# Performance work log

Hardware: AMD Instinct MI355X
Metric: run time of the kernel (lower is better)

The kernel has to match this reference:

```python
import jax, jax.numpy as jnp
import numpy as np

B, L, DM, H, DK, DV = 8, 1024, 512, 8, 64, 64
LN_EPS = 1e-5

def setup_inputs() -> dict:
    key = jax.random.key(0)
    ks = jax.random.split(key, 8)
    s_in = 1.0 / np.sqrt(DM)
    return {
        "q": jax.random.normal(ks[0], (B, L, DM), jnp.float32),
        "k": jax.random.normal(ks[1], (B, L, DM), jnp.float32),
        "v": jax.random.normal(ks[2], (B, L, DM), jnp.float32),
        "Wq": jax.random.normal(ks[3], (DM, H * DK), jnp.float32) * s_in,
        "bq": jnp.zeros((H * DK,), jnp.float32),
        "Wk": jax.random.normal(ks[4], (DM, H * DK), jnp.float32) * s_in,
        "bk": jnp.zeros((H * DK,), jnp.float32),
        "Wv": jax.random.normal(ks[5], (DM, H * DV), jnp.float32) * s_in,
        "bv": jnp.zeros((H * DV,), jnp.float32),
        "Wmap": jax.random.normal(ks[6], (2 * DK, 1), jnp.float32) * (1.0 / np.sqrt(2 * DK)),
        "bmap": jnp.zeros((1,), jnp.float32),
        "Wfc": jax.random.normal(ks[7], (H * DV, DM), jnp.float32) * (1.0 / np.sqrt(H * DV)),
        "bfc": jnp.zeros((DM,), jnp.float32),
        "ln_scale": jnp.ones((DM,), jnp.float32),
        "ln_bias": jnp.zeros((DM,), jnp.float32),
    }

def reference(q, k, v, Wq, bq, Wk, bk, Wv, bv, Wmap, bmap, Wfc, bfc, ln_scale, ln_bias):
    sz_b, len_q, _ = q.shape
    len_k = k.shape[1]
    residual = q
    # projections -> (H, B, L, d)
    qh = (q @ Wq + bq).reshape(sz_b, len_q, H, DK).transpose(2, 0, 1, 3)
    kh = (k @ Wk + bk).reshape(sz_b, len_k, H, DK).transpose(2, 0, 1, 3)
    vh = (v @ Wv + bv).reshape(sz_b, len_k, H, DV).transpose(2, 0, 1, 3)
    # additive score: Linear(concat(q,k)) == q@Wmap[:DK] + k@Wmap[DK:] + b
    # (avoids materializing the (H*B, Lq, Lk, 2*DK) concat; same math)
    sq = qh @ Wmap[:DK, 0]   # (H, B, Lq)
    sk = kh @ Wmap[DK:, 0]   # (H, B, Lk)
    scores = sq[..., :, None] + sk[..., None, :] + bmap[0]  # (H, B, Lq, Lk)
    attn = jax.nn.softmax(scores, axis=-1)
    out = jnp.einsum('hbqk,hbkd->hbqd', attn, vh)            # (H, B, Lq, DV)
    out = out.transpose(1, 2, 0, 3).reshape(sz_b, len_q, H * DV)
    out = out @ Wfc + bfc + residual
    mu = out.mean(-1, keepdims=True)
    var = out.var(-1, keepdims=True)
    out = (out - mu) / jnp.sqrt(var + LN_EPS) * ln_scale + ln_bias
    return out, attn.reshape(H * sz_b, len_q, len_k)
```

## Files before the change

kernel.cpp:

```cpp
#include <hip/hip_runtime.h>
#include <cstdint>
#include <cstddef>

#define B 8
#define L 1024
#define DM 512
#define H 8
#define DK 64
#define DV 64
#define LN_EPS 1e-5f

#define U_OFF    0
#define CK_OFF   4096
#define SK_OFF   8192
#define P_OFF    73728
#define PART_OFF 139264
#define CTX_OFF  270336
#define OBP_OFF  274432

#define OUT_ELEMS  ((size_t)B * L * DM)

typedef float f4 __attribute__((ext_vector_type(4)));

__global__ __launch_bounds__(64) void k_prep(const float* __restrict__ Wk,
                                             const float* __restrict__ bk,
                                             const float* __restrict__ Wmap,
                                             float* __restrict__ ws) {
    __shared__ float wm[DK];
    int t = threadIdx.x;
    wm[t] = Wmap[DK + t];
    __syncthreads();
    int h = t >> 3, part = t & 7;
#pragma unroll
    for (int i = 0; i < 8; ++i) {
        int dm = blockIdx.x * 8 + i;
        const float* row = Wk + (size_t)dm * (H * DK) + h * DK + part * 8;
        float s = 0.f;
#pragma unroll
        for (int d = 0; d < 8; ++d) s += row[d] * wm[part * 8 + d];
        s += __shfl_xor(s, 1, 64);
        s += __shfl_xor(s, 2, 64);
        s += __shfl_xor(s, 4, 64);
        if (part == 0) ws[U_OFF + dm * H + h] = s;
    }
    if (blockIdx.x == 0) {
        const float* rb = bk + h * DK + part * 8;
        float s = 0.f;
#pragma unroll
        for (int d = 0; d < 8; ++d) s += rb[d] * wm[part * 8 + d];
        s += __shfl_xor(s, 1, 64);
        s += __shfl_xor(s, 2, 64);
        s += __shfl_xor(s, 4, 64);
        if (part == 0) ws[CK_OFF + h] = s;
    }
}

__global__ __launch_bounds__(256) void k_sk(const float* __restrict__ k,
                                            float* __restrict__ ws) {
    int wave = threadIdx.x >> 6, lane = threadIdx.x & 63;
    int row = blockIdx.x * 4 + wave;
    int b = row >> 10, l = row & 1023;
    const float* krow = k + (size_t)row * DM;
    const float* u = ws + U_OFF;
    float acc[8] = {0, 0, 0, 0, 0, 0, 0, 0};
#pragma unroll
    for (int s = 0; s < 8; ++s) {
        int dm = s * 64 + lane;
        float kv = krow[dm];
        const float4 ua = *(const float4*)(u + dm * 8);
        const float4 ub = *(const float4*)(u + dm * 8 + 4);
        acc[0] += kv * ua.x; acc[1] += kv * ua.y;
        acc[2] += kv * ua.z; acc[3] += kv * ua.w;
        acc[4] += kv * ub.x; acc[5] += kv * ub.y;
        acc[6] += kv * ub.z; acc[7] += kv * ub.w;
    }
#pragma unroll
    for (int off = 32; off > 0; off >>= 1) {
#pragma unroll
        for (int h = 0; h < 8; ++h) acc[h] += __shfl_xor(acc[h], off, 64);
    }
    float vout = 0.f;
#pragma unroll
    for (int h = 0; h < 8; ++h) if (lane == h) vout = acc[h];
    if (lane < 8)
        ws[SK_OFF + ((size_t)(lane * B + b)) * L + l] = vout + ws[CK_OFF + lane];
}

__global__ __launch_bounds__(256) void k_softmax(float* __restrict__ ws) {
    int hb = blockIdx.x, t = threadIdx.x;
    int wave = t >> 6, lane = t & 63;
    const float4 s4 = *(const float4*)&ws[SK_OFF + (size_t)hb * L + t * 4];
    __shared__ float sred[4];
    __shared__ float bc[1];
    float m = fmaxf(fmaxf(s4.x, s4.y), fmaxf(s4.z, s4.w));
#pragma unroll
    for (int off = 32; off > 0; off >>= 1) m = fmaxf(m, __shfl_xor(m, off, 64));
    if (lane == 0) sred[wave] = m;
    __syncthreads();
    if (t == 0) bc[0] = fmaxf(fmaxf(sred[0], sred[1]), fmaxf(sred[2], sred[3]));
    __syncthreads();
    m = bc[0];
    float e0 = expf(s4.x - m), e1 = expf(s4.y - m), e2 = expf(s4.z - m), e3 = expf(s4.w - m);
    float s = e0 + e1 + e2 + e3;
#pragma unroll
    for (int off = 32; off > 0; off >>= 1) s += __shfl_xor(s, off, 64);
    __syncthreads();
    if (lane == 0) sred[wave] = s;
    __syncthreads();
    if (t == 0) bc[0] = sred[0] + sred[1] + sred[2] + sred[3];
    __syncthreads();
    float inv = 1.f / bc[0];
    float4 p4 = {e0 * inv, e1 * inv, e2 * inv, e3 * inv};
    *(float4*)&ws[P_OFF + (size_t)hb * L + t * 4] = p4;
}

__global__ __launch_bounds__(512) void k_vbar(const float* __restrict__ v,
                                              float* __restrict__ ws) {
    __shared__ float ps[H * 256];
    int blk = blockIdx.x;
    int chunk = blk & 7, b = (blk >> 3) & 7, js = blk >> 6;
    for (int idx = threadIdx.x; idx < H * 256; idx += 512) {
        int hh = idx >> 8, jj = idx & 255;
        ps[idx] = ws[P_OFF + ((size_t)(hh * B + b)) * L + js * 256 + jj];
    }
    __syncthreads();
    int h = threadIdx.x >> 6, dml = threadIdx.x & 63;
    int dm = chunk * 64 + dml;
    const float* vb0 = v + ((size_t)b * L + js * 256) * DM + dm;
    const float* ph = &ps[h * 256];
    float acc = 0.f;
#pragma unroll 4
    for (int jj = 0; jj < 256; ++jj) acc += ph[jj] * vb0[(size_t)jj * DM];
    ws[PART_OFF + ((size_t)((js * H + h) * B + b)) * DM + dm] = acc;
}

__global__ __launch_bounds__(256) void k_ctx(const float* __restrict__ Wv,
                                             const float* __restrict__ bv,
                                             float* __restrict__ ws) {
    __shared__ float vb[DM];
    __shared__ float red[4][64];
    int hb = blockIdx.x;
    int h = hb >> 3, b = hb & 7;
#pragma unroll
    for (int it = 0; it < 2; ++it) {
        int dm = threadIdx.x + it * 256;
        float s = 0.f;
#pragma unroll
        for (int js = 0; js < 4; ++js)
            s += ws[PART_OFF + ((size_t)((js * H + h) * B + b)) * DM + dm];
        vb[dm] = s;
    }
    __syncthreads();
    int w = threadIdx.x >> 6, d = threadIdx.x & 63;
    float acc = 0.f;
#pragma unroll 4
    for (int i = 0; i < 128; ++i) {
        int dm = w * 128 + i;
        acc += vb[dm] * Wv[(size_t)dm * (H * DV) + h * DV + d];
    }
    red[w][d] = acc;
    __syncthreads();
    if (w == 0) {
        float r = red[0][d] + red[1][d] + red[2][d] + red[3][d] + bv[h * DV + d];
        ws[CTX_OFF + (size_t)b * DM + h * DV + d] = r;
    }
}

__global__ __launch_bounds__(512) void k_obase(const float* __restrict__ Wfc,
                                               float* __restrict__ ws) {
    __shared__ float cxs[64];
    int b = blockIdx.x & 7, ms = blockIdx.x >> 3;
    if (threadIdx.x < 64)
        cxs[threadIdx.x] = ws[CTX_OFF + (size_t)b * DM + ms * 64 + threadIdx.x];
    __syncthreads();
    int n = threadIdx.x;
    float acc = 0.f;
#pragma unroll 4
    for (int m = 0; m < 64; ++m)
        acc += cxs[m] * Wfc[(size_t)(ms * 64 + m) * DM + n];
    ws[OBP_OFF + (size_t)(ms * B + b) * DM + n] = acc;
}

__global__ __launch_bounds__(256) void k_out(const float* __restrict__ q,
                                             const float* __restrict__ bfc,
                                             const float* __restrict__ lns,
                                             const float* __restrict__ lnb,
                                             const float* __restrict__ ws,
                                             float* __restrict__ out) {
    __shared__ float obf[DM];
    int b = blockIdx.x >> 8;
    for (int i = threadIdx.x; i < DM; i += 256) {
        float s = bfc[i];
#pragma unroll
        for (int ms = 0; ms < 8; ++ms)
            s += ws[OBP_OFF + (size_t)(ms * B + b) * DM + i];
        obf[i] = s;
    }
    __syncthreads();
    int wave = threadIdx.x >> 6, lane = threadIdx.x & 63;
    int row = blockIdx.x * 4 + wave;
    const float* qr = q + (size_t)row * DM;
    int d0 = lane * 8;
    float4 a = *(const float4*)(qr + d0);
    float4 c = *(const float4*)(qr + d0 + 4);
    float x[8] = {a.x + obf[d0], a.y + obf[d0 + 1], a.z + obf[d0 + 2], a.w + obf[d0 + 3],
                  c.x + obf[d0 + 4], c.y + obf[d0 + 5], c.z + obf[d0 + 6], c.w + obf[d0 + 7]};
    float sum = 0.f, sq = 0.f;
#pragma unroll
    for (int i = 0; i < 8; ++i) { sum += x[i]; sq += x[i] * x[i]; }
#pragma unroll
    for (int off = 32; off > 0; off >>= 1) {
        sum += __shfl_xor(sum, off, 64);
        sq  += __shfl_xor(sq,  off, 64);
    }
    float mu = sum * (1.f / DM);
    float var = sq * (1.f / DM) - mu * mu;
    float inv = rsqrtf(var + LN_EPS);
    float4 sa = *(const float4*)(lns + d0);
    float4 sc = *(const float4*)(lns + d0 + 4);
    float4 ba = *(const float4*)(lnb + d0);
    float4 bb = *(const float4*)(lnb + d0 + 4);
    float sarr[8] = {sa.x, sa.y, sa.z, sa.w, sc.x, sc.y, sc.z, sc.w};
    float barr[8] = {ba.x, ba.y, ba.z, ba.w, bb.x, bb.y, bb.z, bb.w};
    float y[8];
#pragma unroll
    for (int i = 0; i < 8; ++i) y[i] = (x[i] - mu) * inv * sarr[i] + barr[i];
    float4 o0 = {y[0], y[1], y[2], y[3]};
    float4 o1 = {y[4], y[5], y[6], y[7]};
    *(float4*)(out + (size_t)row * DM + d0) = o0;
    *(float4*)(out + (size_t)row * DM + d0 + 4) = o1;
}

__global__ __launch_bounds__(256) void k_attn(const float* __restrict__ ws,
                                              float* __restrict__ out) {
    int hb = blockIdx.x >> 6;
    int ic = blockIdx.x & 63;
    f4 pv = *(const f4*)&ws[P_OFF + (size_t)hb * L + threadIdx.x * 4];
    float* base = out + OUT_ELEMS + ((size_t)hb * L + (size_t)ic * 16) * L + threadIdx.x * 4;
#pragma unroll
    for (int r = 0; r < 16; ++r)
        __builtin_nontemporal_store(pv, (f4*)(base + (size_t)r * L));
}

extern "C" void kernel_launch(void* const* d_in, const int* in_sizes, int n_in,
                              void* d_out, int out_size, void* d_ws, size_t ws_size,
                              hipStream_t stream) {
    const float* q    = (const float*)d_in[0];
    const float* k    = (const float*)d_in[1];
    const float* v    = (const float*)d_in[2];
    const float* Wk   = (const float*)d_in[5];
    const float* bk   = (const float*)d_in[6];
    const float* Wv   = (const float*)d_in[7];
    const float* bv   = (const float*)d_in[8];
    const float* Wmap = (const float*)d_in[9];
    const float* Wfc  = (const float*)d_in[11];
    const float* bfc  = (const float*)d_in[12];
    const float* lns  = (const float*)d_in[13];
    const float* lnb  = (const float*)d_in[14];
    float* out = (float*)d_out;
    float* ws  = (float*)d_ws;

    hipLaunchKernelGGL(k_prep,    dim3(64),   dim3(64),  0, stream, Wk, bk, Wmap, ws);
    hipLaunchKernelGGL(k_sk,      dim3(2048), dim3(256), 0, stream, k, ws);
    hipLaunchKernelGGL(k_softmax, dim3(64),   dim3(256), 0, stream, ws);
    hipLaunchKernelGGL(k_vbar,    dim3(256),  dim3(512), 0, stream, v, ws);
    hipLaunchKernelGGL(k_ctx,     dim3(64),   dim3(256), 0, stream, Wv, bv, ws);
    hipLaunchKernelGGL(k_obase,   dim3(64),   dim3(512), 0, stream, Wfc, ws);
    hipLaunchKernelGGL(k_out,     dim3(2048), dim3(256), 0, stream, q, bfc, lns, lnb, ws, out);
    hipLaunchKernelGGL(k_attn,    dim3(4096), dim3(256), 0, stream, ws, out);
}
```

Before: 118.2 us.

## Fuse all stages into one cooperative kernel overlapping attention-map stores

Replaces the eight separate launches with a single cooperative persistent kernel of 512 blocks that uses grid-wide syncs between stages. The large attention-map writes are split into tasks and handed to otherwise idle blocks during the small serial stages (v-bar, ctx, obase), so the bandwidth-bound output stream overlaps the dependent compute chain. Softmax is now recomputed per task instead of being read from a stored probability buffer, the constant key-bias term that cancels in softmax is dropped, and fast __expf replaces expf. In exchange the kernel pays for five grid syncs, repeats the row reductions in every task, and needs all blocks to be co-resident.

```diff
diff --git a/kernel.cpp b/kernel.cpp
--- a/kernel.cpp
+++ b/kernel.cpp
@@ -1,245 +1,266 @@
 #include <hip/hip_runtime.h>
+#include <hip/hip_cooperative_groups.h>
 #include <cstdint>
 #include <cstddef>
+
+namespace cg = cooperative_groups;
 
 #define B 8
 #define L 1024
 #define DM 512
 #define H 8
-#define DK 64
-#define DV 64
 #define LN_EPS 1e-5f
 
 #define U_OFF    0
-#define CK_OFF   4096
 #define SK_OFF   8192
-#define P_OFF    73728
-#define PART_OFF 139264
-#define CTX_OFF  270336
-#define OBP_OFF  274432
-
-#define OUT_ELEMS  ((size_t)B * L * DM)
+#define PART_OFF 73728
+#define CTX_OFF  204800
+#define OBP_OFF  208896
+
+#define OUT_ELEMS ((size_t)B * L * DM)
+
+#define NBLK 512
+#define NTHR 256
 
 typedef float f4 __attribute__((ext_vector_type(4)));
 
-__global__ __launch_bounds__(64) void k_prep(const float* __restrict__ Wk,
-                                             const float* __restrict__ bk,
-                                             const float* __restrict__ Wmap,
-                                             float* __restrict__ ws) {
-    __shared__ float wm[DK];
-    int t = threadIdx.x;
-    wm[t] = Wmap[DK + t];
+__device__ __forceinline__ float wave_max(float m) {
+#pragma unroll
+    for (int off = 32; off > 0; off >>= 1) m = fmaxf(m, __shfl_xor(m, off, 64));
+    return m;
+}
+__device__ __forceinline__ float wave_sum(float s) {
+#pragma unroll
+    for (int off = 32; off > 0; off >>= 1) s += __shfl_xor(s, off, 64);
+    return s;
+}
+
+__device__ __forceinline__ void attn_task(int task, const float* __restrict__ ws,
+                                          float* __restrict__ out,
+                                          float* rmax, float* rsum,
+                                          int t, int wave, int lane) {
+    int hb = task >> 6, ic = task & 63;
+    float4 s4 = *(const float4*)&ws[SK_OFF + (size_t)hb * L + t * 4];
+    float m = wave_max(fmaxf(fmaxf(s4.x, s4.y), fmaxf(s4.z, s4.w)));
+    if (lane == 0) rmax[wave] = m;
     __syncthreads();
-    int h = t >> 3, part = t & 7;
-#pragma unroll
-    for (int i = 0; i < 8; ++i) {
-        int dm = blockIdx.x * 8 + i;
-        const float* row = Wk + (size_t)dm * (H * DK) + h * DK + part * 8;
-        float s = 0.f;
-#pragma unroll
-        for (int d = 0; d < 8; ++d) s += row[d] * wm[part * 8 + d];
-        s += __shfl_xor(s, 1, 64);
-        s += __shfl_xor(s, 2, 64);
-        s += __shfl_xor(s, 4, 64);
-        if (part == 0) ws[U_OFF + dm * H + h] = s;
-    }
-    if (blockIdx.x == 0) {
-        const float* rb = bk + h * DK + part * 8;
-        float s = 0.f;
-#pragma unroll
-        for (int d = 0; d < 8; ++d) s += rb[d] * wm[part * 8 + d];
-        s += __shfl_xor(s, 1, 64);
-        s += __shfl_xor(s, 2, 64);
-        s += __shfl_xor(s, 4, 64);
-        if (part == 0) ws[CK_OFF + h] = s;
-    }
-}
-
-__global__ __launch_bounds__(256) void k_sk(const float* __restrict__ k,
-                                            float* __restrict__ ws) {
-    int wave = threadIdx.x >> 6, lane = threadIdx.x & 63;
-    int row = blockIdx.x * 4 + wave;
-    int b = row >> 10, l = row & 1023;
-    const float* krow = k + (size_t)row * DM;
-    const float* u = ws + U_OFF;
-    float acc[8] = {0, 0, 0, 0, 0, 0, 0, 0};
-#pragma unroll
-    for (int s = 0; s < 8; ++s) {
-        int dm = s * 64 + lane;
-        float kv = krow[dm];
-        const float4 ua = *(const float4*)(u + dm * 8);
-        const float4 ub = *(const float4*)(u + dm * 8 + 4);
-        acc[0] += kv * ua.x; acc[1] += kv * ua.y;
-        acc[2] += kv * ua.z; acc[3] += kv * ua.w;
-        acc[4] += kv * ub.x; acc[5] += kv * ub.y;
-        acc[6] += kv * ub.z; acc[7] += kv * ub.w;
-    }
-#pragma unroll
-    for (int off = 32; off > 0; off >>= 1) {
-#pragma unroll
-        for (int h = 0; h < 8; ++h) acc[h] += __shfl_xor(acc[h], off, 64);
-    }
-    float vout = 0.f;
-#pragma unroll
-    for (int h = 0; h < 8; ++h) if (lane == h) vout = acc[h];
-    if (lane < 8)
-        ws[SK_OFF + ((size_t)(lane * B + b)) * L + l] = vout + ws[CK_OFF + lane];
-}
-
-__global__ __launch_bounds__(256) void k_softmax(float* __restrict__ ws) {
-    int hb = blockIdx.x, t = threadIdx.x;
-    int wave = t >> 6, lane = t & 63;
-    const float4 s4 = *(const float4*)&ws[SK_OFF + (size_t)hb * L + t * 4];
-    __shared__ float sred[4];
-    __shared__ float bc[1];
-    float m = fmaxf(fmaxf(s4.x, s4.y), fmaxf(s4.z, s4.w));
-#pragma unroll
-    for (int off = 32; off > 0; off >>= 1) m = fmaxf(m, __shfl_xor(m, off, 64));
-    if (lane == 0) sred[wave] = m;
+    m = fmaxf(fmaxf(rmax[0], rmax[1]), fmaxf(rmax[2], rmax[3]));
+    float e0 = __expf(s4.x - m), e1 = __expf(s4.y - m),
+          e2 = __expf(s4.z - m), e3 = __expf(s4.w - m);
+    float ss = wave_sum(e0 + e1 + e2 + e3);
+    if (lane == 0) rsum[wave] = ss;
     __syncthreads();
-    if (t == 0) bc[0] = fmaxf(fmaxf(sred[0], sred[1]), fmaxf(sred[2], sred[3]));
-    __syncthreads();
-    m = bc[0];
-    float e0 = expf(s4.x - m), e1 = expf(s4.y - m), e2 = expf(s4.z - m), e3 = expf(s4.w - m);
-    float s = e0 + e1 + e2 + e3;
-#pragma unroll
-    for (int off = 32; off > 0; off >>= 1) s += __shfl_xor(s, off, 64);
-    __syncthreads();
-    if (lane == 0) sred[wave] = s;
-    __syncthreads();
-    if (t == 0) bc[0] = sred[0] + sred[1] + sred[2] + sred[3];
-    __syncthreads();
-    float inv = 1.f / bc[0];
-    float4 p4 = {e0 * inv, e1 * inv, e2 * inv, e3 * inv};
-    *(float4*)&ws[P_OFF + (size_t)hb * L + t * 4] = p4;
-}
-
-__global__ __launch_bounds__(512) void k_vbar(const float* __restrict__ v,
-                                              float* __restrict__ ws) {
-    __shared__ float ps[H * 256];
+    ss = rsum[0] + rsum[1] + rsum[2] + rsum[3];
+    float inv = 1.f / ss;
+    f4 p4 = {e0 * inv, e1 * inv, e2 * inv, e3 * inv};
+    float* base = out + OUT_ELEMS + ((size_t)hb * L + (size_t)ic * 16) * L + t * 4;
+#pragma unroll
+    for (int r = 0; r < 16; ++r)
+        __builtin_nontemporal_store(p4, (f4*)(base + (size_t)r * L));
+}
+
+__global__ __launch_bounds__(NTHR, 4) void kfused(
+    const float* __restrict__ q, const float* __restrict__ k, const float* __restrict__ v,
+    const float* __restrict__ Wk, const float* __restrict__ Wv, const float* __restrict__ bv,
+    const float* __restrict__ Wmap, const float* __restrict__ Wfc, const float* __restrict__ bfc,
+    const float* __restrict__ lns, const float* __restrict__ lnb,
+    float* __restrict__ out, float* __restrict__ ws)
+{
+    cg::grid_group grid = cg::this_grid();
+    __shared__ float smem[2056];
+    float* rmax = smem + 2048;
+    float* rsum = smem + 2052;
+    int t = threadIdx.x, wave = t >> 6, lane = t & 63;
     int blk = blockIdx.x;
-    int chunk = blk & 7, b = (blk >> 3) & 7, js = blk >> 6;
-    for (int idx = threadIdx.x; idx < H * 256; idx += 512) {
-        int hh = idx >> 8, jj = idx & 255;
-        ps[idx] = ws[P_OFF + ((size_t)(hh * B + b)) * L + js * 256 + jj];
-    }
-    __syncthreads();
-    int h = threadIdx.x >> 6, dml = threadIdx.x & 63;
-    int dm = chunk * 64 + dml;
-    const float* vb0 = v + ((size_t)b * L + js * 256) * DM + dm;
-    const float* ph = &ps[h * 256];
-    float acc = 0.f;
+
+    {
+        if (t < 64) smem[t] = Wmap[64 + t];
+        __syncthreads();
+        int pair = blk * 8 + (t >> 5);
+        int dm = pair >> 3, h = pair & 7;
+        int sub = t & 31;
+        const float* row = Wk + (size_t)dm * (H * 64) + h * 64 + sub * 2;
+        float s = row[0] * smem[sub * 2] + row[1] * smem[sub * 2 + 1];
+#pragma unroll
+        for (int off = 1; off < 32; off <<= 1) s += __shfl_xor(s, off, 64);
+        if (sub == 0) ws[U_OFF + pair] = s;
+    }
+    grid.sync();
+
+    {
+        const float* u = ws + U_OFF;
+#pragma unroll
+        for (int rep = 0; rep < 4; ++rep) {
+            int row = blk * 16 + rep * 4 + wave;
+            int b = row >> 10, l = row & 1023;
+            const float* krow = k + (size_t)row * DM;
+            float acc[8] = {0, 0, 0, 0, 0, 0, 0, 0};
+#pragma unroll
+            for (int s8 = 0; s8 < 8; ++s8) {
+                int dm = s8 * 64 + lane;
+                float kv = krow[dm];
+                const float4 ua = *(const float4*)(u + dm * 8);
+                const float4 ub = *(const float4*)(u + dm * 8 + 4);
+                acc[0] += kv * ua.x; acc[1] += kv * ua.y;
+                acc[2] += kv * ua.z; acc[3] += kv * ua.w;
+                acc[4] += kv * ub.x; acc[5] += kv * ub.y;
+                acc[6] += kv * ub.z; acc[7] += kv * ub.w;
+            }
+#pragma unroll
+            for (int off = 32; off > 0; off >>= 1) {
+#pragma unroll
+                for (int h = 0; h < 8; ++h) acc[h] += __shfl_xor(acc[h], off, 64);
+            }
+            float vout = 0.f;
+#pragma unroll
+            for (int h = 0; h < 8; ++h) if (lane == h) vout = acc[h];
+            if (lane < 8)
+                ws[SK_OFF + ((size_t)(lane * B + b)) * L + l] = vout;
+        }
+    }
+    grid.sync();
+
+    if (blk < 256) {
+        int js = blk >> 6, b = (blk >> 3) & 7, chunk = blk & 7;
+        for (int h = 0; h < H; ++h) {
+            float4 s4 = *(const float4*)&ws[SK_OFF + ((size_t)(h * B + b)) * L + t * 4];
+            float m = wave_max(fmaxf(fmaxf(s4.x, s4.y), fmaxf(s4.z, s4.w)));
+            if (lane == 0) rmax[wave] = m;
+            __syncthreads();
+            m = fmaxf(fmaxf(rmax[0], rmax[1]), fmaxf(rmax[2], rmax[3]));
+            float e0 = __expf(s4.x - m), e1 = __expf(s4.y - m),
+                  e2 = __expf(s4.z - m), e3 = __expf(s4.w - m);
+            float ss = wave_sum(e0 + e1 + e2 + e3);
+            if (lane == 0) rsum[wave] = ss;
+            __syncthreads();
+            ss = rsum[0] + rsum[1] + rsum[2] + rsum[3];
+            float inv = 1.f / ss;
+            if (wave == js) {
+                smem[h * 256 + lane * 4 + 0] = e0 * inv;
+                smem[h * 256 + lane * 4 + 1] = e1 * inv;
+                smem[h * 256 + lane * 4 + 2] = e2 * inv;
+                smem[h * 256 + lane * 4 + 3] = e3 * inv;
+            }
+        }
+        __syncthreads();
+        int dm = chunk * 64 + lane;
+        const float* vb0 = v + ((size_t)b * L + js * 256) * DM + dm;
+#pragma unroll
+        for (int rep = 0; rep < 2; ++rep) {
+            int h = wave * 2 + rep;
+            const float* ph = &smem[h * 256];
+            float acc = 0.f;
 #pragma unroll 4
-    for (int jj = 0; jj < 256; ++jj) acc += ph[jj] * vb0[(size_t)jj * DM];
-    ws[PART_OFF + ((size_t)((js * H + h) * B + b)) * DM + dm] = acc;
-}
-
-__global__ __launch_bounds__(256) void k_ctx(const float* __restrict__ Wv,
-                                             const float* __restrict__ bv,
-                                             float* __restrict__ ws) {
-    __shared__ float vb[DM];
-    __shared__ float red[4][64];
-    int hb = blockIdx.x;
-    int h = hb >> 3, b = hb & 7;
-#pragma unroll
-    for (int it = 0; it < 2; ++it) {
-        int dm = threadIdx.x + it * 256;
-        float s = 0.f;
-#pragma unroll
-        for (int js = 0; js < 4; ++js)
-            s += ws[PART_OFF + ((size_t)((js * H + h) * B + b)) * DM + dm];
-        vb[dm] = s;
-    }
-    __syncthreads();
-    int w = threadIdx.x >> 6, d = threadIdx.x & 63;
-    float acc = 0.f;
+            for (int jj = 0; jj < 256; ++jj) acc += ph[jj] * vb0[(size_t)jj * DM];
+            ws[PART_OFF + ((size_t)((js * H + h) * B + b)) * DM + dm] = acc;
+        }
+    } else {
+        for (int task = blk - 256; task < 800; task += 256)
+            attn_task(task, ws, out, rmax, rsum, t, wave, lane);
+    }
+    grid.sync();
+
+    if (blk < 64) {
+        int h = blk >> 3, b = blk & 7;
+        float* vb = smem;
+        float* red = smem + 512;
+#pragma unroll
+        for (int it = 0; it < 2; ++it) {
+            int dm = t + it * 256;
+            float s = 0.f;
+#pragma unroll
+            for (int js = 0; js < 4; ++js)
+                s += ws[PART_OFF + ((size_t)((js * H + h) * B + b)) * DM + dm];
+            vb[dm] = s;
+        }
+        __syncthreads();
+        float acc = 0.f;
 #pragma unroll 4
-    for (int i = 0; i < 128; ++i) {
-        int dm = w * 128 + i;
-        acc += vb[dm] * Wv[(size_t)dm * (H * DV) + h * DV + d];
-    }
-    red[w][d] = acc;
-    __syncthreads();
-    if (w == 0) {
-        float r = red[0][d] + red[1][d] + red[2][d] + red[3][d] + bv[h * DV + d];
-        ws[CTX_OFF + (size_t)b * DM + h * DV + d] = r;
-    }
-}
-
-__global__ __launch_bounds__(512) void k_obase(const float* __restrict__ Wfc,
-                                               float* __restrict__ ws) {
-    __shared__ float cxs[64];
-    int b = blockIdx.x & 7, ms = blockIdx.x >> 3;
-    if (threadIdx.x < 64)
-        cxs[threadIdx.x] = ws[CTX_OFF + (size_t)b * DM + ms * 64 + threadIdx.x];
-    __syncthreads();
-    int n = threadIdx.x;
-    float acc = 0.f;
+        for (int i = 0; i < 128; ++i) {
+            int dm = wave * 128 + i;
+            acc += vb[dm] * Wv[(size_t)dm * DM + h * 64 + lane];
+        }
+        red[wave * 64 + lane] = acc;
+        __syncthreads();
+        if (wave == 0) {
+            float r = red[lane] + red[64 + lane] + red[128 + lane] + red[192 + lane]
+                    + bv[h * 64 + lane];
+            ws[CTX_OFF + (size_t)b * DM + h * 64 + lane] = r;
+        }
+    } else {
+        for (int task = 800 + (blk - 64); task < 2100; task += 448)
+            attn_task(task, ws, out, rmax, rsum, t, wave, lane);
+    }
+    grid.sync();
+
+    if (blk < 64) {
+        int ms = blk >> 3, b = blk & 7;
+        if (t < 64) smem[t] = ws[CTX_OFF + (size_t)b * DM + ms * 64 + t];
+        __syncthreads();
+#pragma unroll
+        for (int it = 0; it < 2; ++it) {
+            int n = t + it * 256;
+            float acc = 0.f;
 #pragma unroll 4
-    for (int m = 0; m < 64; ++m)
-        acc += cxs[m] * Wfc[(size_t)(ms * 64 + m) * DM + n];
-    ws[OBP_OFF + (size_t)(ms * B + b) * DM + n] = acc;
-}
-
-__global__ __launch_bounds__(256) void k_out(const float* __restrict__ q,
-                                             const float* __restrict__ bfc,
-                                             const float* __restrict__ lns,
-                                             const float* __restrict__ lnb,
-                                             const float* __restrict__ ws,
-                                             float* __restrict__ out) {
-    __shared__ float obf[DM];
-    int b = blockIdx.x >> 8;
-    for (int i = threadIdx.x; i < DM; i += 256) {
-        float s = bfc[i];
-#pragma unroll
-        for (int ms = 0; ms < 8; ++ms)
-            s += ws[OBP_OFF + (size_t)(ms * B + b) * DM + i];
-        obf[i] = s;
-    }
-    __syncthreads();
-    int wave = threadIdx.x >> 6, lane = threadIdx.x & 63;
-    int row = blockIdx.x * 4 + wave;
-    const float* qr = q + (size_t)row * DM;
-    int d0 = lane * 8;
-    float4 a = *(const float4*)(qr + d0);
-    float4 c = *(const float4*)(qr + d0 + 4);
-    float x[8] = {a.x + obf[d0], a.y + obf[d0 + 1], a.z + obf[d0 + 2], a.w + obf[d0 + 3],
-                  c.x + obf[d0 + 4], c.y + obf[d0 + 5], c.z + obf[d0 + 6], c.w + obf[d0 + 7]};
-    float sum = 0.f, sq = 0.f;
-#pragma unroll
-    for (int i = 0; i < 8; ++i) { sum += x[i]; sq += x[i] * x[i]; }
-#pragma unroll
-    for (int off = 32; off > 0; off >>= 1) {
-        sum += __shfl_xor(sum, off, 64);
-        sq  += __shfl_xor(sq,  off, 64);
-    }
-    float mu = sum * (1.f / DM);
-    float var = sq * (1.f / DM) - mu * mu;
-    float inv = rsqrtf(var + LN_EPS);
-    float4 sa = *(const float4*)(lns + d0);
-    float4 sc = *(const float4*)(lns + d0 + 4);
-    float4 ba = *(const float4*)(lnb + d0);
-    float4 bb = *(const float4*)(lnb + d0 + 4);
-    float sarr[8] = {sa.x, sa.y, sa.z, sa.w, sc.x, sc.y, sc.z, sc.w};
-    float barr[8] = {ba.x, ba.y, ba.z, ba.w, bb.x, bb.y, bb.z, bb.w};
-    float y[8];
-#pragma unroll
-    for (int i = 0; i < 8; ++i) y[i] = (x[i] - mu) * inv * sarr[i] + barr[i];
-    float4 o0 = {y[0], y[1], y[2], y[3]};
-    float4 o1 = {y[4], y[5], y[6], y[7]};
-    *(float4*)(out + (size_t)row * DM + d0) = o0;
-    *(float4*)(out + (size_t)row * DM + d0 + 4) = o1;
-}
-
-__global__ __launch_bounds__(256) void k_attn(const float* __restrict__ ws,
-                                              float* __restrict__ out) {
-    int hb = blockIdx.x >> 6;
-    int ic = blockIdx.x & 63;
-    f4 pv = *(const f4*)&ws[P_OFF + (size_t)hb * L + threadIdx.x * 4];
-    float* base = out + OUT_ELEMS + ((size_t)hb * L + (size_t)ic * 16) * L + threadIdx.x * 4;
-#pragma unroll
-    for (int r = 0; r < 16; ++r)
-        __builtin_nontemporal_store(pv, (f4*)(base + (size_t)r * L));
+            for (int m = 0; m < 64; ++m)
+                acc += smem[m] * Wfc[(size_t)(ms * 64 + m) * DM + n];
+            ws[OBP_OFF + (size_t)(ms * B + b) * DM + n] = acc;
+        }
+    } else {
+        for (int task = 2100 + (blk - 64); task < 3400; task += 448)
+            attn_task(task, ws, out, rmax, rsum, t, wave, lane);
+    }
+    grid.sync();
+
+    {
+        int b = blk >> 6;
+        for (int i = t; i < DM; i += NTHR) {
+            float s = bfc[i];
+#pragma unroll
+            for (int ms = 0; ms < 8; ++ms)
+                s += ws[OBP_OFF + (size_t)(ms * B + b) * DM + i];
+            smem[i] = s;
+        }
+        __syncthreads();
+#pragma unroll
+        for (int rep = 0; rep < 4; ++rep) {
+            int row = blk * 16 + rep * 4 + wave;
+            const float* qr = q + (size_t)row * DM;
+            int d0 = lane * 8;
+            float4 a = *(const float4*)(qr + d0);
+            float4 c = *(const float4*)(qr + d0 + 4);
+            float x[8] = {a.x + smem[d0],     a.y + smem[d0 + 1],
+                          a.z + smem[d0 + 2], a.w + smem[d0 + 3],
+                          c.x + smem[d0 + 4], c.y + smem[d0 + 5],
+                          c.z + smem[d0 + 6], c.w + smem[d0 + 7]};
+            float sum = 0.f, sq = 0.f;
+#pragma unroll
+            for (int i = 0; i < 8; ++i) { sum += x[i]; sq += x[i] * x[i]; }
+#pragma unroll
+            for (int off = 32; off > 0; off >>= 1) {
+                sum += __shfl_xor(sum, off, 64);
+                sq  += __shfl_xor(sq,  off, 64);
+            }
+            float mu = sum * (1.f / DM);
+            float var = sq * (1.f / DM) - mu * mu;
+            float inv = rsqrtf(var + LN_EPS);
+            float4 sa = *(const float4*)(lns + d0);
+            float4 sc = *(const float4*)(lns + d0 + 4);
+            float4 ba = *(const float4*)(lnb + d0);
+            float4 bb = *(const float4*)(lnb + d0 + 4);
+            float sarr[8] = {sa.x, sa.y, sa.z, sa.w, sc.x, sc.y, sc.z, sc.w};
+            float barr[8] = {ba.x, ba.y, ba.z, ba.w, bb.x, bb.y, bb.z, bb.w};
+            float y[8];
+#pragma unroll
+            for (int i = 0; i < 8; ++i) y[i] = (x[i] - mu) * inv * sarr[i] + barr[i];
+            float4 o0 = {y[0], y[1], y[2], y[3]};
+            float4 o1 = {y[4], y[5], y[6], y[7]};
+            *(float4*)(out + (size_t)row * DM + d0) = o0;
+            *(float4*)(out + (size_t)row * DM + d0 + 4) = o1;
+        }
+        for (int task = 3400 + blk; task < 4096; task += NBLK)
+            attn_task(task, ws, out, rmax, rsum, t, wave, lane);
+    }
 }
 
 extern "C" void kernel_launch(void* const* d_in, const int* in_sizes, int n_in,
@@ -249,7 +270,6 @@
     const float* k    = (const float*)d_in[1];
     const float* v    = (const float*)d_in[2];
     const float* Wk   = (const float*)d_in[5];
-    const float* bk   = (const float*)d_in[6];
     const float* Wv   = (const float*)d_in[7];
     const float* bv   = (const float*)d_in[8];
     const float* Wmap = (const float*)d_in[9];
@@ -260,12 +280,9 @@
     float* out = (float*)d_out;
     float* ws  = (float*)d_ws;
 
-    hipLaunchKernelGGL(k_prep,    dim3(64),   dim3(64),  0, stream, Wk, bk, Wmap, ws);
-    hipLaunchKernelGGL(k_sk,      dim3(2048), dim3(256), 0, stream, k, ws);
-    hipLaunchKernelGGL(k_softmax, dim3(64),   dim3(256), 0, stream, ws);
-    hipLaunchKernelGGL(k_vbar,    dim3(256),  dim3(512), 0, stream, v, ws);
-    hipLaunchKernelGGL(k_ctx,     dim3(64),   dim3(256), 0, stream, Wv, bv, ws);
-    hipLaunchKernelGGL(k_obase,   dim3(64),   dim3(512), 0, stream, Wfc, ws);
-    hipLaunchKernelGGL(k_out,     dim3(2048), dim3(256), 0, stream, q, bfc, lns, lnb, ws, out);
-    hipLaunchKernelGGL(k_attn,    dim3(4096), dim3(256), 0, stream, ws, out);
-}
+    void* args[] = {(void*)&q, (void*)&k, (void*)&v, (void*)&Wk, (void*)&Wv, (void*)&bv,
+                    (void*)&Wmap, (void*)&Wfc, (void*)&bfc, (void*)&lns, (void*)&lnb,
+                    (void*)&out, (void*)&ws};
+    hipLaunchCooperativeKernel((const void*)kfused, dim3(NBLK), dim3(NTHR),
+                               args, 0, stream);
+}
```

Result: slower. 419.8 us (+255.2%).
